# Kernel tuning notes

Hardware: AMD Instinct MI355X
Metric: run time of the kernel (lower is better)

The kernel has to match this reference:

```python
import jax, jax.numpy as jnp
import numpy as np

N_NODES = 10000
N_EDGES = 160000
IN_C, HID_C, OUT_C = 256, 512, 256
DROP_P = 0.5


def setup_inputs() -> dict:
    key = jax.random.key(0)
    ks = jax.random.split(key, 6)
    tensor = jax.random.normal(ks[0], (N_NODES, IN_C), dtype=jnp.float32)
    edge_index = jax.random.randint(ks[1], (2, N_EDGES), 0, N_NODES, dtype=jnp.int64)
    # Glorot-ish init for GCNConv linear weights, zero bias (PyG default bias init is zeros)
    W1 = jax.random.normal(ks[2], (IN_C, HID_C), dtype=jnp.float32) * (1.0 / np.sqrt(IN_C))
    b1 = jnp.zeros((HID_C,), dtype=jnp.float32)
    W2 = jax.random.normal(ks[3], (HID_C, OUT_C), dtype=jnp.float32) * (1.0 / np.sqrt(HID_C))
    b2 = jnp.zeros((OUT_C,), dtype=jnp.float32)
    return {"tensor": tensor, "edge_index": edge_index, "W1": W1, "b1": b1, "W2": W2, "b2": b2}


def _gcn_layer(x, W, b, src, dst, n_nodes):
    # x' = D^{-1/2} (A + I) D^{-1/2} X W + b  (PyG GCNConv, add_self_loops=True)
    xw = x @ W                                             # [N, C_out]
    deg = jax.ops.segment_sum(jnp.ones(src.shape[0], xw.dtype), dst,
                              num_segments=n_nodes)        # includes self-loops -> deg >= 1
    dinv = jax.lax.rsqrt(deg)
    norm = dinv[src] * dinv[dst]                           # [E+N]
    msg = xw[src] * norm[:, None]                          # gather + normalize
    out = jax.ops.segment_sum(msg, dst, num_segments=n_nodes)  # scatter-add
    return out + b


def _dropout(x, key, p):
    keep = jax.random.bernoulli(key, 1.0 - p, x.shape)
    return jnp.where(keep, x / (1.0 - p), jnp.zeros((), x.dtype))


def reference(tensor, edge_index, W1, b1, W2, b2):
    n = tensor.shape[0]
    src, dst = edge_index[0], edge_index[1]
    loops = jnp.arange(n, dtype=src.dtype)
    src_f = jnp.concatenate([src, loops])
    dst_f = jnp.concatenate([dst, loops])

    dk1, dk2 = jax.random.split(jax.random.key(42))
    h = _gcn_layer(tensor, W1, b1, src_f, dst_f, n)
    h = jax.nn.relu(h)
    h = _dropout(h, dk1, DROP_P)
    h = _gcn_layer(h, W2, b2, src_f, dst_f, n)
    h = jax.nn.relu(h)
    h = _dropout(h, dk2, DROP_P)
    return h
```

## Files before the change

### kernel.cpp

```cpp
#include <hip/hip_runtime.h>
#include <stdint.h>


#define C_IN 256
#define C_HID 512
#define C_OUT 256

typedef unsigned short ushort_t;
typedef __bf16 bf16x8 __attribute__((ext_vector_type(8)));
typedef float floatx4 __attribute__((ext_vector_type(4)));

__host__ __device__ __forceinline__ void tf_rounds(unsigned& x0, unsigned& x1,
                                                   unsigned k0, unsigned k1) {
  unsigned k2 = k0 ^ k1 ^ 0x1BD11BDAu;
#define ROT(r) { x0 += x1; x1 = (x1 << r) | (x1 >> (32 - r)); x1 ^= x0; }
  x0 += k0; x1 += k1;
  ROT(13) ROT(15) ROT(26) ROT(6)
  x0 += k1; x1 += k2 + 1u;
  ROT(17) ROT(29) ROT(16) ROT(24)
  x0 += k2; x1 += k0 + 2u;
  ROT(13) ROT(15) ROT(26) ROT(6)
  x0 += k0; x1 += k1 + 3u;
  ROT(17) ROT(29) ROT(16) ROT(24)
  x0 += k1; x1 += k2 + 4u;
  ROT(13) ROT(15) ROT(26) ROT(6)
  x0 += k2; x1 += k0 + 5u;
#undef ROT
}

__device__ __forceinline__ float drop_scale(unsigned j, unsigned k0, unsigned k1) {
  unsigned x0 = 0u, x1 = j;
  tf_rounds(x0, x1, k0, k1);
  unsigned bits = x0 ^ x1;
  float u = __uint_as_float((bits >> 9) | 0x3f800000u) - 1.0f;
  return (u < 0.5f) ? 2.0f : 0.0f;
}

__device__ __forceinline__ ushort_t f2bf(float f) {
  unsigned u = __float_as_uint(f);
  unsigned r = (u + 0x7fffu + ((u >> 16) & 1u)) >> 16;
  return (ushort_t)r;
}
__device__ __forceinline__ float bf2f(ushort_t h) {
  return __uint_as_float(((unsigned)h) << 16);
}

__global__ __launch_bounds__(256) void k_setup(const unsigned* __restrict__ raw,
                                               unsigned* flag, int nwords,
                                               int* __restrict__ cnt, int n,
                                               int nb) {
  if ((int)blockIdx.x < nb) {
    int i = blockIdx.x * 256 + threadIdx.x;
    if (i < n) cnt[i] = 0;
    return;
  }
  __shared__ unsigned sh[256];
  unsigned acc = 0;
  for (int i = 1 + 2 * (int)threadIdx.x; i < nwords; i += 512) acc |= raw[i];
  sh[threadIdx.x] = acc;
  __syncthreads();
  for (int s = 128; s > 0; s >>= 1) {
    if ((int)threadIdx.x < s) sh[threadIdx.x] |= sh[threadIdx.x + s];
    __syncthreads();
  }
  if (threadIdx.x == 0) *flag = (sh[0] == 0u) ? 1u : 0u;
}

__global__ __launch_bounds__(256) void k_convert(const void* __restrict__ raw,
                                                 const unsigned* __restrict__ flag,
                                                 int* __restrict__ eic,
                                                 int* __restrict__ cnt,
                                                 int E) {
  int i = blockIdx.x * 256 + threadIdx.x;
  if (i >= 2 * E) return;
  int v;
  if (*flag) v = (int)((const long long*)raw)[i];
  else       v = ((const int*)raw)[i];
  eic[i] = v;
  if (i >= E) atomicAdd(&cnt[v], 1);
}

#define SCAN_CH 16
__global__ __launch_bounds__(1024) void k_scan1(const int* __restrict__ cnt,
                                                int* __restrict__ roff,
                                                int* __restrict__ cursor,
                                                float* __restrict__ dinv, int n) {
  __shared__ int sh[1024];
  const int t = threadIdx.x;
  const int base = t * SCAN_CH;
  int vv[SCAN_CH], loc[SCAN_CH];
  int sum = 0;
#pragma unroll
  for (int i = 0; i < SCAN_CH; ++i) {
    int idx = base + i;
    int v = (idx < n) ? cnt[idx] : 0;
    vv[i] = v;
    loc[i] = sum;
    sum += v;
  }
  sh[t] = sum;
  __syncthreads();
  for (int s = 1; s < 1024; s <<= 1) {
    int v = (t >= s) ? sh[t - s] : 0;
    __syncthreads();
    sh[t] += v;
    __syncthreads();
  }
  int tex = sh[t] - sum;
#pragma unroll
  for (int i = 0; i < SCAN_CH; ++i) {
    int idx = base + i;
    if (idx < n) {
      int excl = tex + loc[i];
      roff[idx] = excl;
      cursor[idx] = excl;
      dinv[idx] = rsqrtf((float)(vv[i] + 1));
    }
  }
  if (t == 1023) roff[n] = sh[1023];
}

__global__ __launch_bounds__(256) void k_scat_wconv(
    const int* __restrict__ eic, int* __restrict__ cursor,
    const float* __restrict__ dinv, int2* __restrict__ csrw, int E, int SB,
    const float* __restrict__ W1, const float* __restrict__ W2,
    ushort_t* __restrict__ h1, ushort_t* __restrict__ l1,
    ushort_t* __restrict__ h2, ushort_t* __restrict__ l2) {
  int b = blockIdx.x;
  if (b < SB) {
    int e = b * 256 + threadIdx.x;
    if (e >= E) return;
    int s = eic[e], d = eic[E + e];
    int slot = atomicAdd(&cursor[d], 1);
    int2 val;
    val.x = s;
    val.y = __float_as_int(dinv[s]);
    csrw[slot] = val;
    return;
  }
  int idx = (b - SB) * 256 + threadIdx.x;
  const int S1 = C_IN * C_HID;
  const int S2 = C_HID * C_OUT;
  if (idx >= S1 + S2) return;
  const float* W; ushort_t *hi, *lo; int K, Nn, li;
  if (idx < S1) { W = W1; hi = h1; lo = l1; K = C_IN; Nn = C_HID; li = idx; }
  else { W = W2; hi = h2; lo = l2; K = C_HID; Nn = C_OUT; li = idx - S1; }
  int k = li / Nn, n = li - k * Nn;
  float v = W[li];
  ushort_t h = f2bf(v);
  hi[(size_t)n * K + k] = h;
  lo[(size_t)n * K + k] = f2bf(v - bf2f(h));
}

template <int EPI>
__global__ __launch_bounds__(256) void k_gather4(const int* __restrict__ roff,
                                                 const int2* __restrict__ csrw,
                                                 const float* __restrict__ dinv,
                                                 const float* __restrict__ x,
                                                 const float* __restrict__ bias,
                                                 void* __restrict__ o1,
                                                 void* __restrict__ o2,
                                                 unsigned dk0, unsigned dk1) {
  const int g = threadIdx.x >> 6;
  const int lane = threadIdx.x & 63;
  const int node = blockIdx.x * 4 + g;
  float dd = dinv[node];
  float4 v = ((const float4*)(x + (size_t)node * 256))[lane];
  float4 acc = make_float4(dd * v.x, dd * v.y, dd * v.z, dd * v.w);
  int p = roff[node], end = roff[node + 1];
  while (p < end) {
    int2 ew[8];
#pragma unroll
    for (int i = 0; i < 8; ++i) {
      int q = p + i;
      ew[i] = csrw[q < end ? q : (end - 1)];
    }
#pragma unroll
    for (int i = 0; i < 8; ++i) {
      float w = (p + i < end) ? __int_as_float(ew[i].y) : 0.0f;
      float4 a = ((const float4*)(x + (size_t)ew[i].x * 256))[lane];
      acc.x += w * a.x;
      acc.y += w * a.y;
      acc.z += w * a.z;
      acc.w += w * a.w;
    }
    p += 8;
  }
  acc.x *= dd; acc.y *= dd; acc.z *= dd; acc.w *= dd;
  if (EPI) {
    float4 bb = ((const float4*)bias)[lane];
    acc.x = fmaxf(acc.x + bb.x, 0.0f);
    acc.y = fmaxf(acc.y + bb.y, 0.0f);
    acc.z = fmaxf(acc.z + bb.z, 0.0f);
    acc.w = fmaxf(acc.w + bb.w, 0.0f);
    unsigned jb = (unsigned)node * 256u + (unsigned)lane * 4u;
    acc.x *= drop_scale(jb + 0u, dk0, dk1);
    acc.y *= drop_scale(jb + 1u, dk0, dk1);
    acc.z *= drop_scale(jb + 2u, dk0, dk1);
    acc.w *= drop_scale(jb + 3u, dk0, dk1);
    ((float4*)o1)[(size_t)node * 64 + lane] = acc;
  } else {
    ushort_t h0 = f2bf(acc.x), h1 = f2bf(acc.y), h2 = f2bf(acc.z), h3 = f2bf(acc.w);
    ushort4 hv = make_ushort4(h0, h1, h2, h3);
    ushort4 lv = make_ushort4(f2bf(acc.x - bf2f(h0)), f2bf(acc.y - bf2f(h1)),
                              f2bf(acc.z - bf2f(h2)), f2bf(acc.w - bf2f(h3)));
    ((ushort4*)o1)[(size_t)node * 64 + lane] = hv;
    ((ushort4*)o2)[(size_t)node * 64 + lane] = lv;
  }
}

template <int EPI>
__global__ __launch_bounds__(256) void k_gemm3(
    const ushort_t* __restrict__ Ahi, const ushort_t* __restrict__ Alo,
    const ushort_t* __restrict__ Bhi, const ushort_t* __restrict__ Blo,
    const float* __restrict__ bias,
    ushort_t* __restrict__ Chi, ushort_t* __restrict__ Clo,
    float* __restrict__ Cf,
    int M, int N, int K, unsigned dk0, unsigned dk1) {
  __shared__ ushort_t sAh[128 * 32], sAl[128 * 32], sBh[128 * 32], sBl[128 * 32];
  const int t = threadIdx.x;
  const int lane = t & 63, wave = t >> 6;
  const int wm = wave & 1, wn = wave >> 1;
  const int quad = lane >> 4, l16 = lane & 15;
  const int row0 = blockIdx.y * 128, col0 = blockIdx.x * 128;
  const int srow = t >> 2;
  const int skc = (t & 3) * 8;

  floatx4 acc[4][4] = {};

  const int ra0 = min(row0 + srow, M - 1);
  const int ra1 = min(row0 + 64 + srow, M - 1);
  const int rb0 = col0 + srow;
  const int rb1 = col0 + 64 + srow;

  for (int kt = 0; kt < K; kt += 32) {
    const size_t ka = (size_t)kt + skc;
    uint4 vA0h = *(const uint4*)(Ahi + (size_t)ra0 * K + ka);
    uint4 vA1h = *(const uint4*)(Ahi + (size_t)ra1 * K + ka);
    uint4 vA0l = *(const uint4*)(Alo + (size_t)ra0 * K + ka);
    uint4 vA1l = *(const uint4*)(Alo + (size_t)ra1 * K + ka);
    uint4 vB0h = *(const uint4*)(Bhi + (size_t)rb0 * K + ka);
    uint4 vB1h = *(const uint4*)(Bhi + (size_t)rb1 * K + ka);
    uint4 vB0l = *(const uint4*)(Blo + (size_t)rb0 * K + ka);
    uint4 vB1l = *(const uint4*)(Blo + (size_t)rb1 * K + ka);
    __syncthreads();
    *(uint4*)&sAh[srow * 32 + skc] = vA0h;
    *(uint4*)&sAh[(64 + srow) * 32 + skc] = vA1h;
    *(uint4*)&sAl[srow * 32 + skc] = vA0l;
    *(uint4*)&sAl[(64 + srow) * 32 + skc] = vA1l;
    *(uint4*)&sBh[srow * 32 + skc] = vB0h;
    *(uint4*)&sBh[(64 + srow) * 32 + skc] = vB1h;
    *(uint4*)&sBl[srow * 32 + skc] = vB0l;
    *(uint4*)&sBl[(64 + srow) * 32 + skc] = vB1l;
    __syncthreads();

    bf16x8 ah[4], al[4], bh[4], bl[4];
#pragma unroll
    for (int i = 0; i < 4; ++i) {
      int off = (wm * 64 + i * 16 + l16) * 32 + quad * 8;
      ah[i] = *(const bf16x8*)&sAh[off];
      al[i] = *(const bf16x8*)&sAl[off];
    }
#pragma unroll
    for (int j = 0; j < 4; ++j) {
      int off = (wn * 64 + j * 16 + l16) * 32 + quad * 8;
      bh[j] = *(const bf16x8*)&sBh[off];
      bl[j] = *(const bf16x8*)&sBl[off];
    }
#pragma unroll
    for (int i = 0; i < 4; ++i)
#pragma unroll
      for (int j = 0; j < 4; ++j) {
        acc[i][j] = __builtin_amdgcn_mfma_f32_16x16x32_bf16(ah[i], bh[j], acc[i][j], 0, 0, 0);
        acc[i][j] = __builtin_amdgcn_mfma_f32_16x16x32_bf16(ah[i], bl[j], acc[i][j], 0, 0, 0);
        acc[i][j] = __builtin_amdgcn_mfma_f32_16x16x32_bf16(al[i], bh[j], acc[i][j], 0, 0, 0);
      }
  }

#pragma unroll
  for (int i = 0; i < 4; ++i) {
#pragma unroll
    for (int j = 0; j < 4; ++j) {
      int gc = col0 + wn * 64 + j * 16 + l16;
#pragma unroll
      for (int reg = 0; reg < 4; ++reg) {
        int gr = row0 + wm * 64 + i * 16 + quad * 4 + reg;
        if (gr >= M) continue;
        float v = acc[i][j][reg];
        size_t o = (size_t)gr * N + gc;
        if (EPI) {
          v += bias[gc];
          v = fmaxf(v, 0.0f);
          v *= drop_scale((unsigned)gr * (unsigned)N + (unsigned)gc, dk0, dk1);
          ushort_t h = f2bf(v);
          Chi[o] = h;
          Clo[o] = f2bf(v - bf2f(h));
        } else {
          Cf[o] = v;
        }
      }
    }
  }
}

extern "C" void kernel_launch(void* const* d_in, const int* in_sizes, int n_in,
                              void* d_out, int out_size, void* d_ws, size_t ws_size,
                              hipStream_t stream) {
  const float* x  = (const float*)d_in[0];
  const void*  ei = d_in[1];
  const float* W1 = (const float*)d_in[2];
  const float* b1 = (const float*)d_in[3];
  const float* W2 = (const float*)d_in[4];
  const float* b2 = (const float*)d_in[5];
  float* out = (float*)d_out;

  const int N = in_sizes[0] / C_IN;
  const int E = in_sizes[1] / 2;
  const int NB = (N + 255) / 256;

  unsigned a0 = 0u, a1 = 0u, b0 = 0u, b1k = 1u;
  tf_rounds(a0, a1, 0u, 42u);
  tf_rounds(b0, b1k, 0u, 42u);

  uintptr_t base = (uintptr_t)d_ws;
  unsigned*  flag   = (unsigned*)base;
  int*       cnt    = (int*)(base + 16 * 1024);
  int*       roff   = (int*)(base + 64 * 1024);
  int*       cursor = (int*)(base + 128 * 1024);
  float*     dinv   = (float*)(base + 192 * 1024);
  int*       eic    = (int*)(base + 256 * 1024);
  int2*      csrw   = (int2*)(base + 2u * 1024 * 1024);
  ushort_t*  Ahi    = (ushort_t*)(base + 4u  * 1024 * 1024);
  ushort_t*  Alo    = (ushort_t*)(base + 10u * 1024 * 1024);
  ushort_t*  H1hi   = (ushort_t*)(base + 16u * 1024 * 1024);
  ushort_t*  H1lo   = (ushort_t*)(base + 27u * 1024 * 1024);
  float*     hw2    = (float*)(base + 38u * 1024 * 1024);
  ushort_t*  W1thi  = (ushort_t*)(base + 49u * 1024 * 1024);
  ushort_t*  W1tlo  = (ushort_t*)(base + 49u * 1024 * 1024 + 512 * 1024);
  ushort_t*  W2thi  = (ushort_t*)(base + 50u * 1024 * 1024);
  ushort_t*  W2tlo  = (ushort_t*)(base + 50u * 1024 * 1024 + 512 * 1024);

  dim3 b256(256);
  const int SB = (E + 255) / 256;
  const int WB = (C_IN * C_HID + C_HID * C_OUT + 255) / 256;

  k_setup<<<dim3(NB + 1), b256, 0, stream>>>((const unsigned*)ei, flag, 8192, cnt, N, NB);
  k_convert<<<dim3((2 * E + 255) / 256), b256, 0, stream>>>(ei, flag, eic, cnt, E);
  k_scan1<<<dim3(1), dim3(1024), 0, stream>>>(cnt, roff, cursor, dinv, N);
  k_scat_wconv<<<dim3(SB + WB), b256, 0, stream>>>(eic, cursor, dinv, csrw, E, SB,
                                                   W1, W2, W1thi, W1tlo, W2thi, W2tlo);
  k_gather4<0><<<dim3(N / 4), b256, 0, stream>>>(roff, csrw, dinv, x, nullptr,
                                                 Ahi, Alo, 0u, 0u);
  k_gemm3<1><<<dim3(C_HID / 128, (N + 127) / 128), b256, 0, stream>>>(
      Ahi, Alo, W1thi, W1tlo, b1, H1hi, H1lo, nullptr, N, C_HID, C_IN, a0, a1);
  k_gemm3<0><<<dim3(C_OUT / 128, (N + 127) / 128), b256, 0, stream>>>(
      H1hi, H1lo, W2thi, W2tlo, nullptr, nullptr, nullptr, hw2, N, C_OUT, C_HID, 0u, 0u);
  k_gather4<1><<<dim3(N / 4), b256, 0, stream>>>(roff, csrw, dinv, hw2, b2,
                                                 out, nullptr, b0, b1k);
}
```

Measured before the change: 223.5 us.

## Load GEMM tiles directly to LDS and split gather loop into full/tail chunks

The GEMM tile staging now uses global_load_lds intrinsics to copy 16-byte chunks straight from global memory into shared memory, skipping the register round-trip and the separate LDS stores. Each wave writes a contiguous 512-element region, which matches the previous per-thread layout (srow*32+skc). The gather kernel's edge loop is split into an unpredicated 8-wide main loop and a scalar tail, removing the clamped index and weight masking on every edge. Risks: the direct-to-LDS path needs correct wait counts before the barrier and offers no double-buffering overlap. The tail loop also issues serial loads for leftover edges.

```diff
diff --git a/kernel.cpp b/kernel.cpp
--- a/kernel.cpp
+++ b/kernel.cpp
@@ -9,6 +9,12 @@
 typedef unsigned short ushort_t;
 typedef __bf16 bf16x8 __attribute__((ext_vector_type(8)));
 typedef float floatx4 __attribute__((ext_vector_type(4)));
+
+__device__ __forceinline__ void gload_lds16(const void* g, void* l) {
+  __builtin_amdgcn_global_load_lds(
+      (const __attribute__((address_space(1))) unsigned*)g,
+      (__attribute__((address_space(3))) unsigned*)l, 16, 0, 0);
+}
 
 __host__ __device__ __forceinline__ void tf_rounds(unsigned& x0, unsigned& x1,
                                                    unsigned k0, unsigned k1) {
@@ -168,23 +174,22 @@
   float4 v = ((const float4*)(x + (size_t)node * 256))[lane];
   float4 acc = make_float4(dd * v.x, dd * v.y, dd * v.z, dd * v.w);
   int p = roff[node], end = roff[node + 1];
-  while (p < end) {
+  for (; p + 8 <= end; p += 8) {
     int2 ew[8];
 #pragma unroll
+    for (int i = 0; i < 8; ++i) ew[i] = csrw[p + i];
+#pragma unroll
     for (int i = 0; i < 8; ++i) {
-      int q = p + i;
-      ew[i] = csrw[q < end ? q : (end - 1)];
-    }
-#pragma unroll
-    for (int i = 0; i < 8; ++i) {
-      float w = (p + i < end) ? __int_as_float(ew[i].y) : 0.0f;
+      float w = __int_as_float(ew[i].y);
       float4 a = ((const float4*)(x + (size_t)ew[i].x * 256))[lane];
-      acc.x += w * a.x;
-      acc.y += w * a.y;
-      acc.z += w * a.z;
-      acc.w += w * a.w;
-    }
-    p += 8;
+      acc.x += w * a.x; acc.y += w * a.y; acc.z += w * a.z; acc.w += w * a.w;
+    }
+  }
+  for (; p < end; ++p) {
+    int2 e = csrw[p];
+    float w = __int_as_float(e.y);
+    float4 a = ((const float4*)(x + (size_t)e.x * 256))[lane];
+    acc.x += w * a.x; acc.y += w * a.y; acc.z += w * a.z; acc.w += w * a.w;
   }
   acc.x *= dd; acc.y *= dd; acc.z *= dd; acc.w *= dd;
   if (EPI) {
@@ -225,6 +230,7 @@
   const int row0 = blockIdx.y * 128, col0 = blockIdx.x * 128;
   const int srow = t >> 2;
   const int skc = (t & 3) * 8;
+  const int wbase = wave * 512;
 
   floatx4 acc[4][4] = {};
 
@@ -235,23 +241,15 @@
 
   for (int kt = 0; kt < K; kt += 32) {
     const size_t ka = (size_t)kt + skc;
-    uint4 vA0h = *(const uint4*)(Ahi + (size_t)ra0 * K + ka);
-    uint4 vA1h = *(const uint4*)(Ahi + (size_t)ra1 * K + ka);
-    uint4 vA0l = *(const uint4*)(Alo + (size_t)ra0 * K + ka);
-    uint4 vA1l = *(const uint4*)(Alo + (size_t)ra1 * K + ka);
-    uint4 vB0h = *(const uint4*)(Bhi + (size_t)rb0 * K + ka);
-    uint4 vB1h = *(const uint4*)(Bhi + (size_t)rb1 * K + ka);
-    uint4 vB0l = *(const uint4*)(Blo + (size_t)rb0 * K + ka);
-    uint4 vB1l = *(const uint4*)(Blo + (size_t)rb1 * K + ka);
-    __syncthreads();
-    *(uint4*)&sAh[srow * 32 + skc] = vA0h;
-    *(uint4*)&sAh[(64 + srow) * 32 + skc] = vA1h;
-    *(uint4*)&sAl[srow * 32 + skc] = vA0l;
-    *(uint4*)&sAl[(64 + srow) * 32 + skc] = vA1l;
-    *(uint4*)&sBh[srow * 32 + skc] = vB0h;
-    *(uint4*)&sBh[(64 + srow) * 32 + skc] = vB1h;
-    *(uint4*)&sBl[srow * 32 + skc] = vB0l;
-    *(uint4*)&sBl[(64 + srow) * 32 + skc] = vB1l;
+    __syncthreads();
+    gload_lds16(Ahi + (size_t)ra0 * K + ka, &sAh[wbase]);
+    gload_lds16(Ahi + (size_t)ra1 * K + ka, &sAh[2048 + wbase]);
+    gload_lds16(Alo + (size_t)ra0 * K + ka, &sAl[wbase]);
+    gload_lds16(Alo + (size_t)ra1 * K + ka, &sAl[2048 + wbase]);
+    gload_lds16(Bhi + (size_t)rb0 * K + ka, &sBh[wbase]);
+    gload_lds16(Bhi + (size_t)rb1 * K + ka, &sBh[2048 + wbase]);
+    gload_lds16(Blo + (size_t)rb0 * K + ka, &sBl[wbase]);
+    gload_lds16(Blo + (size_t)rb1 * K + ka, &sBl[2048 + wbase]);
     __syncthreads();
 
     bf16x8 ah[4], al[4], bh[4], bl[4];
```

Result: no change. 227.1 us (+1.6%).
